# Kernel tuning notes

Hardware: AMD Instinct MI355X
Metric: run time of the kernel (lower is better)

The kernel has to match this reference:

```python
import jax, jax.numpy as jnp
import numpy as np

B, N, M, C, S = 4, 16384, 128, 128, 512  # batch, points, boxes, feat dim, sampled pts


def setup_inputs() -> dict:
    key = jax.random.key(0)
    k1, k2, k3, k4, k5, k6, k7 = jax.random.split(key, 7)
    # point cloud roughly in a LiDAR extent
    xy = jax.random.uniform(k1, (B, N, 2), minval=-50.0, maxval=50.0)
    z = jax.random.uniform(k2, (B, N, 1), minval=-3.0, maxval=3.0)
    points = jnp.concatenate([xy, z], axis=-1).astype(jnp.float32)
    point_features = jax.random.normal(k3, (B, N, C), dtype=jnp.float32)
    # boxes: (cx, cy, cz_bottom, dx, dy, dz, rz)
    ctr_xy = jax.random.uniform(k4, (B, M, 2), minval=-50.0, maxval=50.0)
    ctr_z = jax.random.uniform(k5, (B, M, 1), minval=-3.0, maxval=0.0)
    sizes = jax.random.uniform(k6, (B, M, 3), minval=2.0, maxval=8.0)
    rz = jax.random.uniform(k7, (B, M, 1), minval=-np.pi, maxval=np.pi)
    boxes3d = jnp.concatenate([ctr_xy, ctr_z, sizes, rz], axis=-1).astype(jnp.float32)
    return {"points": points, "point_features": point_features, "boxes3d": boxes3d}


def _pool_one_box(points, feats, box):
    # points (N,3), feats (N,C), box (7,)
    n = points.shape[0]
    cx, cy, cz, dx, dy, dz, rz = box
    cz = cz + 0.5 * dz  # bottom center -> geometric center (mmcv convention)
    sx = points[:, 0] - cx
    sy = points[:, 1] - cy
    cosa = jnp.cos(-rz)
    sina = jnp.sin(-rz)
    lx = sx * cosa - sy * sina
    ly = sx * sina + sy * cosa
    mask = (
        (jnp.abs(points[:, 2] - cz) <= 0.5 * dz)
        & (lx > -0.5 * dx) & (lx < 0.5 * dx)
        & (ly > -0.5 * dy) & (ly < 0.5 * dy)
    )
    cnt = mask.sum(dtype=jnp.int32)
    # rank of each in-box point among in-box points (first-come order)
    rank = jnp.cumsum(mask.astype(jnp.int32)) - 1
    pos = jnp.where(mask, rank, n)  # out-of-range for non-members -> dropped
    table = jnp.zeros((n,), jnp.int32).at[pos].set(
        jnp.arange(n, dtype=jnp.int32), mode="drop")
    # wrap-around duplication when cnt < S (kernel copies k % cnt)
    j = jnp.arange(S, dtype=jnp.int32) % jnp.maximum(cnt, 1)
    idx = table[j]  # (S,)
    pooled = jnp.concatenate([points[idx], feats[idx]], axis=-1)  # (S, 3+C)
    pooled = jnp.where(cnt > 0, pooled, jnp.zeros_like(pooled))
    empty = (cnt == 0).astype(jnp.int32)
    return pooled, empty


def reference(points, point_features, boxes3d):
    # vmap over boxes, then over batch
    per_scene = jax.vmap(_pool_one_box, in_axes=(None, None, 0))
    per_batch = jax.vmap(per_scene, in_axes=(0, 0, 0))
    pooled_features, pooled_empty_flag = per_batch(points, point_features, boxes3d)
    return pooled_features, pooled_empty_flag
```

## Files before the change

kernel.cpp:

```cpp
#include <hip/hip_runtime.h>

#define B_ 4
#define N_ 16384
#define M_ 128
#define C_ 128
#define S_ 512
#define ROW_ 131
#define NCHUNK_ 256
#define TILE_ 128
#define LSTR_ 136
#define KBOX_ 4

typedef float f4_t __attribute__((ext_vector_type(4)));

__device__ __forceinline__ int swz(int j, int col) {
    return j * LSTR_ + (col & 3) * 34 + (col >> 2);
}

__global__ __launch_bounds__(256) void mask_kernel(
    const float* __restrict__ points,
    const float* __restrict__ boxes,
    unsigned long long* __restrict__ masks)
{
    const int gwave = blockIdx.x * 4 + (threadIdx.x >> 6);
    const int lane  = threadIdx.x & 63;
    const int grp   = gwave >> 4;
    const int seg   = gwave & 15;
    const int bm0   = grp * KBOX_;
    const int b     = bm0 >> 7;

    const float* pb = points + (size_t)b * N_ * 3;
    float px[16], py[16], pz[16];
    #pragma unroll
    for (int k = 0; k < 16; ++k) {
        const int i = (seg * 16 + k) * 64 + lane;
        px[k] = pb[i*3+0]; py[k] = pb[i*3+1]; pz[k] = pb[i*3+2];
    }

    for (int kb = 0; kb < KBOX_; ++kb) {
        const int bm = bm0 + kb;
        const float* bx = boxes + bm * 7;
        const float cx = bx[0], cy = bx[1], czb = bx[2];
        const float dx = bx[3], dy = bx[4], dzv = bx[5], rz = bx[6];
        const float cz   = __fadd_rn(czb, __fmul_rn(0.5f, dzv));
        const float cosa = (float)cos(-(double)rz);
        const float sina = (float)sin(-(double)rz);
        const float hdx = 0.5f * dx, hdy = 0.5f * dy, hdz = 0.5f * dzv;

        #pragma unroll
        for (int k = 0; k < 16; ++k) {
            const float sx = __fsub_rn(px[k], cx);
            const float sy = __fsub_rn(py[k], cy);
            const float lx = __fsub_rn(__fmul_rn(sx, cosa), __fmul_rn(sy, sina));
            const float ly = __fadd_rn(__fmul_rn(sx, sina), __fmul_rn(sy, cosa));
            const bool pred = (fabsf(__fsub_rn(pz[k], cz)) <= hdz) &&
                              (lx > -hdx) && (lx < hdx) &&
                              (ly > -hdy) && (ly < hdy);
            const unsigned long long m = __ballot(pred);
            if (lane == 0) masks[(size_t)bm * NCHUNK_ + seg * 16 + k] = m;
        }
    }
}

__global__ __launch_bounds__(256) void pool_kernel(
    const float* __restrict__ points,
    const float* __restrict__ feats,
    const unsigned long long* __restrict__ masks,
    float* __restrict__ out,
    float* __restrict__ flags_out)
{
    const int bm   = blockIdx.x;
    const int b    = bm >> 7;
    const int tid  = threadIdx.x;
    const int w    = tid >> 6;
    const int lane = tid & 63;

    __shared__ int   s_wsum[4];
    __shared__ int   s_idx[S_];
    __shared__ int   jtab[S_ + 1];
    __shared__ float srow[TILE_ * LSTR_];

    const unsigned long long m0 = masks[(size_t)bm * NCHUNK_ + tid];
    const int c = __popcll(m0);

    int incl = c;
    #pragma unroll
    for (int d = 1; d < 64; d <<= 1) {
        const int t = __shfl_up(incl, d, 64);
        if (lane >= d) incl += t;
    }
    if (lane == 63) s_wsum[w] = incl;
    __syncthreads();
    const int w0 = s_wsum[0], w1 = s_wsum[1], w2 = s_wsum[2], w3 = s_wsum[3];
    const int woff  = (w > 0 ? w0 : 0) + (w > 1 ? w1 : 0) + (w > 2 ? w2 : 0);
    const int total = w0 + w1 + w2 + w3;
    const int P = incl - c + woff;

    if (c > 0 && P < S_) {
        unsigned long long m = m0;
        int pos = P;
        while (m && pos < S_) {
            const int bit = __ffsll((unsigned long long)m) - 1;
            m &= m - 1;
            s_idx[pos++] = tid * 64 + bit;
        }
    }
    __syncthreads();

    const int cnt_eff = total < S_ ? total : S_;
    const int denom   = cnt_eff > 0 ? cnt_eff : 1;
    for (int s = tid; s <= S_; s += 256) jtab[s] = (s < S_) ? (s % denom) : 0;

    const int T = cnt_eff < TILE_ ? cnt_eff : TILE_;
    if (total == 0) {
        if (tid < LSTR_) srow[tid] = 0.0f;
    } else {
        const int nf4 = T * 32;
        for (int t = tid; t < nf4; t += 256) {
            const int u = t >> 5, q = t & 31;
            const size_t pbase = (size_t)b * N_ + (unsigned)s_idx[u];
            const f4_t v = *(const f4_t*)(feats + pbase * C_ + q * 4);
            #pragma unroll
            for (int jj = 0; jj < 4; ++jj)
                srow[swz(u, 3 + 4 * q + jj)] = v[jj];
        }
        for (int t = tid; t < T * 3; t += 256) {
            const int u = t / 3, k = t - u * 3;
            const size_t pbase = (size_t)b * N_ + (unsigned)s_idx[u];
            srow[swz(u, k)] = points[pbase * 3 + k];
        }
    }
    __syncthreads();

    float* ob = out + (size_t)bm * (S_ * ROW_);
    if (cnt_eff <= TILE_) {
        for (int f = tid; f < (S_ * ROW_) / 4; f += 256) {
            const int e = 4 * f;
            const unsigned s0 = (unsigned)e / (unsigned)ROW_;
            const int col0 = e - (int)s0 * ROW_;
            const int ja = jtab[s0], jb = jtab[s0 + 1];
            f4_t v;
            #pragma unroll
            for (int jj = 0; jj < 4; ++jj) {
                int col = col0 + jj;
                const bool cross = col >= ROW_;
                col = cross ? col - ROW_ : col;
                const int j = cross ? jb : ja;
                v[jj] = srow[swz(j, col)];
            }
            *(f4_t*)(ob + e) = v;
        }
    } else {
        for (int f = tid; f < (S_ * ROW_) / 4; f += 256) {
            const int e = 4 * f;
            const unsigned s0 = (unsigned)e / (unsigned)ROW_;
            const int col0 = e - (int)s0 * ROW_;
            f4_t v;
            #pragma unroll
            for (int jj = 0; jj < 4; ++jj) {
                int col = col0 + jj;
                unsigned s = s0;
                if (col >= ROW_) { col -= ROW_; ++s; }
                const int j = jtab[s];
                float val;
                if (j < TILE_) {
                    val = srow[swz(j, col)];
                } else {
                    const size_t pbase = (size_t)b * N_ + (unsigned)s_idx[j];
                    val = (col < 3) ? points[pbase * 3 + col]
                                    : feats[pbase * C_ + (col - 3)];
                }
                v[jj] = val;
            }
            *(f4_t*)(ob + e) = v;
        }
    }
    if (tid == 0) flags_out[bm] = (total == 0) ? 1.0f : 0.0f;
}

extern "C" void kernel_launch(void* const* d_in, const int* in_sizes, int n_in,
                              void* d_out, int out_size, void* d_ws, size_t ws_size,
                              hipStream_t stream) {
    const float* points = (const float*)d_in[0];
    const float* feats  = (const float*)d_in[1];
    const float* boxes  = (const float*)d_in[2];
    float* out = (float*)d_out;

    unsigned long long* masks = (unsigned long long*)d_ws;

    float* flags = out + (size_t)B_ * M_ * S_ * ROW_;

    mask_kernel<<<B_ * M_ * 16 / 4 / KBOX_, 256, 0, stream>>>(
        points, boxes, masks);
    pool_kernel<<<B_ * M_, 256, 0, stream>>>(points, feats, masks, out, flags);
}
```

Baseline: 174.0 us.

## Write pooled rows per wavefront with scalar stores and 512-thread blocks

The pool kernel moves to 512 threads per block. The per-element jtab/float4 output loop, with its division by ROW, is replaced by a scheme where each wavefront writes whole 131-float output rows as coalesced scalar stores, using an unswizzled LDS row layout with stride 132. The mask scan still runs on the first 256 threads only. The aim is to drop the per-element index math and the jtab table and to raise parallelism for the store-bound output phase. In exchange it uses scalar instead of vector stores, and rows starting at unaligned 131-float offsets may split cache lines.

```diff
diff --git a/kernel.cpp b/kernel.cpp
--- a/kernel.cpp
+++ b/kernel.cpp
@@ -8,14 +8,10 @@
 #define ROW_ 131
 #define NCHUNK_ 256
 #define TILE_ 128
-#define LSTR_ 136
+#define LSTR2_ 132
 #define KBOX_ 4
 
 typedef float f4_t __attribute__((ext_vector_type(4)));
-
-__device__ __forceinline__ int swz(int j, int col) {
-    return j * LSTR_ + (col & 3) * 34 + (col >> 2);
-}
 
 __global__ __launch_bounds__(256) void mask_kernel(
     const float* __restrict__ points,
@@ -62,7 +58,7 @@
     }
 }
 
-__global__ __launch_bounds__(256) void pool_kernel(
+__global__ __launch_bounds__(512, 4) void pool_kernel(
     const float* __restrict__ points,
     const float* __restrict__ feats,
     const unsigned long long* __restrict__ masks,
@@ -77,102 +73,101 @@
 
     __shared__ int   s_wsum[4];
     __shared__ int   s_idx[S_];
-    __shared__ int   jtab[S_ + 1];
-    __shared__ float srow[TILE_ * LSTR_];
+    __shared__ float srow[TILE_ * LSTR2_];
 
-    const unsigned long long m0 = masks[(size_t)bm * NCHUNK_ + tid];
-    const int c = __popcll(m0);
-
-    int incl = c;
-    #pragma unroll
-    for (int d = 1; d < 64; d <<= 1) {
-        const int t = __shfl_up(incl, d, 64);
-        if (lane >= d) incl += t;
+    unsigned long long m0 = 0;
+    int c = 0, Ppart = 0;
+    if (tid < 256) {
+        m0 = masks[(size_t)bm * NCHUNK_ + tid];
+        c  = __popcll(m0);
+        int incl = c;
+        #pragma unroll
+        for (int d = 1; d < 64; d <<= 1) {
+            const int t = __shfl_up(incl, d, 64);
+            if (lane >= d) incl += t;
+        }
+        if (lane == 63) s_wsum[w] = incl;
+        Ppart = incl - c;
     }
-    if (lane == 63) s_wsum[w] = incl;
     __syncthreads();
     const int w0 = s_wsum[0], w1 = s_wsum[1], w2 = s_wsum[2], w3 = s_wsum[3];
-    const int woff  = (w > 0 ? w0 : 0) + (w > 1 ? w1 : 0) + (w > 2 ? w2 : 0);
     const int total = w0 + w1 + w2 + w3;
-    const int P = incl - c + woff;
 
-    if (c > 0 && P < S_) {
-        unsigned long long m = m0;
-        int pos = P;
-        while (m && pos < S_) {
-            const int bit = __ffsll((unsigned long long)m) - 1;
-            m &= m - 1;
-            s_idx[pos++] = tid * 64 + bit;
+    if (tid < 256 && c > 0) {
+        const int woff = (w > 0 ? w0 : 0) + (w > 1 ? w1 : 0) + (w > 2 ? w2 : 0);
+        int pos = Ppart + woff;
+        if (pos < S_) {
+            unsigned long long m = m0;
+            while (m && pos < S_) {
+                const int bit = __ffsll((unsigned long long)m) - 1;
+                m &= m - 1;
+                s_idx[pos++] = tid * 64 + bit;
+            }
         }
     }
     __syncthreads();
 
     const int cnt_eff = total < S_ ? total : S_;
     const int denom   = cnt_eff > 0 ? cnt_eff : 1;
-    for (int s = tid; s <= S_; s += 256) jtab[s] = (s < S_) ? (s % denom) : 0;
 
     const int T = cnt_eff < TILE_ ? cnt_eff : TILE_;
     if (total == 0) {
-        if (tid < LSTR_) srow[tid] = 0.0f;
+        if (tid < LSTR2_) srow[tid] = 0.0f;
     } else {
         const int nf4 = T * 32;
-        for (int t = tid; t < nf4; t += 256) {
+        for (int t = tid; t < nf4; t += 512) {
             const int u = t >> 5, q = t & 31;
             const size_t pbase = (size_t)b * N_ + (unsigned)s_idx[u];
             const f4_t v = *(const f4_t*)(feats + pbase * C_ + q * 4);
             #pragma unroll
             for (int jj = 0; jj < 4; ++jj)
-                srow[swz(u, 3 + 4 * q + jj)] = v[jj];
+                srow[u * LSTR2_ + 3 + 4 * q + jj] = v[jj];
         }
-        for (int t = tid; t < T * 3; t += 256) {
+        for (int t = tid; t < T * 3; t += 512) {
             const int u = t / 3, k = t - u * 3;
             const size_t pbase = (size_t)b * N_ + (unsigned)s_idx[u];
-            srow[swz(u, k)] = points[pbase * 3 + k];
+            srow[u * LSTR2_ + k] = points[pbase * 3 + k];
         }
     }
     __syncthreads();
 
     float* ob = out + (size_t)bm * (S_ * ROW_);
     if (cnt_eff <= TILE_) {
-        for (int f = tid; f < (S_ * ROW_) / 4; f += 256) {
-            const int e = 4 * f;
-            const unsigned s0 = (unsigned)e / (unsigned)ROW_;
-            const int col0 = e - (int)s0 * ROW_;
-            const int ja = jtab[s0], jb = jtab[s0 + 1];
-            f4_t v;
-            #pragma unroll
-            for (int jj = 0; jj < 4; ++jj) {
-                int col = col0 + jj;
-                const bool cross = col >= ROW_;
-                col = cross ? col - ROW_ : col;
-                const int j = cross ? jb : ja;
-                v[jj] = srow[swz(j, col)];
-            }
-            *(f4_t*)(ob + e) = v;
+        #pragma unroll 2
+        for (int k = 0; k < 64; ++k) {
+            const int s = w + 8 * k;
+            const int j = (int)((unsigned)s % (unsigned)denom);
+            const float* r = srow + j * LSTR2_;
+            const float a = r[lane];
+            const float d2 = r[64 + lane];
+            const float d3 = (lane < 3) ? r[128 + lane] : 0.0f;
+            float* orow = ob + s * ROW_;
+            orow[lane]      = a;
+            orow[64 + lane] = d2;
+            if (lane < 3) orow[128 + lane] = d3;
         }
     } else {
-        for (int f = tid; f < (S_ * ROW_) / 4; f += 256) {
-            const int e = 4 * f;
-            const unsigned s0 = (unsigned)e / (unsigned)ROW_;
-            const int col0 = e - (int)s0 * ROW_;
-            f4_t v;
-            #pragma unroll
-            for (int jj = 0; jj < 4; ++jj) {
-                int col = col0 + jj;
-                unsigned s = s0;
-                if (col >= ROW_) { col -= ROW_; ++s; }
-                const int j = jtab[s];
-                float val;
-                if (j < TILE_) {
-                    val = srow[swz(j, col)];
-                } else {
-                    const size_t pbase = (size_t)b * N_ + (unsigned)s_idx[j];
-                    val = (col < 3) ? points[pbase * 3 + col]
-                                    : feats[pbase * C_ + (col - 3)];
-                }
-                v[jj] = val;
+        #pragma unroll 2
+        for (int k = 0; k < 64; ++k) {
+            const int s = w + 8 * k;
+            const int j = (int)((unsigned)s % (unsigned)denom);
+            float a, d2, d3 = 0.0f;
+            if (j < TILE_) {
+                const float* r = srow + j * LSTR2_;
+                a  = r[lane];
+                d2 = r[64 + lane];
+                if (lane < 3) d3 = r[128 + lane];
+            } else {
+                const size_t pbase = (size_t)b * N_ + (unsigned)s_idx[j];
+                const float* fr = feats + pbase * C_;
+                a  = (lane < 3) ? points[pbase * 3 + lane] : fr[lane - 3];
+                d2 = fr[61 + lane];
+                if (lane < 3) d3 = fr[125 + lane];
             }
-            *(f4_t*)(ob + e) = v;
+            float* orow = ob + s * ROW_;
+            orow[lane]      = a;
+            orow[64 + lane] = d2;
+            if (lane < 3) orow[128 + lane] = d3;
         }
     }
     if (tid == 0) flags_out[bm] = (total == 0) ? 1.0f : 0.0f;
@@ -192,5 +187,5 @@
 
     mask_kernel<<<B_ * M_ * 16 / 4 / KBOX_, 256, 0, stream>>>(
         points, boxes, masks);
-    pool_kernel<<<B_ * M_, 256, 0, stream>>>(points, feats, masks, out, flags);
+    pool_kernel<<<B_ * M_, 512, 0, stream>>>(points, feats, masks, out, flags);
 }
```

Result: no change. 175.8 us (+1.0%).
